# Optimization experiments

Hardware: AMD Instinct MI355X
Metric: run time of the kernel (lower is better)

## Reference

```python
import jax, jax.numpy as jnp
import numpy as np

NEG_SLOPE = 0.2  # PyG GATConv default LeakyReLU slope


def _gat_conv(x, edge_index, W, a_src, a_dst, bias, heads, out_dim, concat):
    """PyG-style GATConv (eval mode, add_self_loops=True).
    x: [N, F_in], edge_index: [2, E] (row=src, col=dst)."""
    N = x.shape[0]
    loops = jnp.tile(jnp.arange(N, dtype=edge_index.dtype)[None, :], (2, 1))
    ei = jnp.concatenate([edge_index, loops], axis=1)  # [2, E+N]
    src, dst = ei[0], ei[1]

    h = (x @ W).reshape(N, heads, out_dim)            # [N, H, D]
    alpha_s = jnp.einsum('nhd,hd->nh', h, a_src)       # [N, H]
    alpha_d = jnp.einsum('nhd,hd->nh', h, a_dst)       # [N, H]

    e = jax.nn.leaky_relu(alpha_s[src] + alpha_d[dst], NEG_SLOPE)  # [E', H]
    # segment softmax over edges grouped by destination node
    m = jax.ops.segment_max(e, dst, num_segments=N)
    e = jnp.exp(e - jax.lax.stop_gradient(m)[dst])
    denom = jax.ops.segment_sum(e, dst, num_segments=N)
    alpha = e / denom[dst]                              # [E', H]

    msg = h[src] * alpha[..., None]                     # [E', H, D]
    out = jax.ops.segment_sum(msg, dst, num_segments=N) # [N, H, D]
    out = out.reshape(N, heads * out_dim) if concat else out.mean(axis=1)
    return out + bias


def setup_inputs() -> dict:
    key = jax.random.key(0)
    ks = jax.random.split(key, 12)
    N, E, F_in, H, D = 50000, 1600000, 64, 2, 32
    s = 0.1
    return {
        'x': jax.random.normal(ks[0], (N, F_in), jnp.float32),
        'edge_index': jax.random.randint(ks[1], (2, E), 0, N, jnp.int64 if jax.config.jax_enable_x64 else jnp.int32),
        'W1': jax.random.normal(ks[2], (F_in, H * D), jnp.float32) * s,
        'a_src1': jax.random.normal(ks[3], (H, D), jnp.float32) * s,
        'a_dst1': jax.random.normal(ks[4], (H, D), jnp.float32) * s,
        'b1': jnp.zeros((H * D,), jnp.float32),
        'W2': jax.random.normal(ks[5], (H * D, D), jnp.float32) * s,
        'a_src2': jax.random.normal(ks[6], (1, D), jnp.float32) * s,
        'a_dst2': jax.random.normal(ks[7], (1, D), jnp.float32) * s,
        'b2': jnp.zeros((D,), jnp.float32),
        'fcW': jax.random.normal(ks[8], (D, 1), jnp.float32) * s,
        'fcb': jnp.zeros((1,), jnp.float32),
    }


def reference(x, edge_index, W1, a_src1, a_dst1, b1, W2, a_src2, a_dst2, b2, fcW, fcb):
    H, D = 2, 32
    h = _gat_conv(x, edge_index, W1, a_src1, a_dst1, b1, heads=H, out_dim=D, concat=True)
    h = jax.nn.elu(h)
    # dropout p=0.1 is a no-op in eval mode
    h = _gat_conv(h, edge_index, W2, a_src2, a_dst2, b2, heads=1, out_dim=D, concat=False)
    h = jax.nn.elu(h)
    scores = h @ fcW + fcb
    return (scores, h)
```

## Files before the change

### kernel.cpp

```cpp
#include <hip/hip_runtime.h>
#include <hip/hip_fp16.h>

#define NEG_SLOPE 0.2f
#define NRANGE 8
#define CAP 96

__device__ __forceinline__ float elu_f(float x) {
    return x > 0.f ? x : __expf(x) - 1.f;
}
__device__ __forceinline__ float lrelu_f(float x) {
    return fmaxf(x, NEG_SLOPE * x);
}

union H4 { float2 f2; __half2 h2[2]; };

__global__ __launch_bounds__(256) void scat_gemm1_kernel(
    const int* __restrict__ ei, int* __restrict__ cnt,
    unsigned short* __restrict__ srclist, int E, int N,
    int nScat, int nChunks,
    const float* __restrict__ x, const float* __restrict__ W1,
    const float* __restrict__ a_src, const float* __restrict__ a_dst,
    __half* __restrict__ h1, float* __restrict__ as1, float* __restrict__ ad1)
{
    __shared__ float Xl[4][64];
    int b = blockIdx.x;
    if (b < 7 * nScat && (b % 7) == 0) {
        int hid = b / 7;
        int range = hid & (NRANGE - 1);
        int chunk = hid >> 3;
        int RS = (N + NRANGE - 1) / NRANGE;
        int lo = range * RS;
        unsigned span = (unsigned)(((lo + RS) > N ? N : (lo + RS)) - lo);
        int per = (E + nChunks - 1) / nChunks;
        int beg = chunk * per;
        int end = beg + per; if (end > E) end = E;
        for (int i = beg + (int)threadIdx.x; i < end; i += 256) {
            int dst = ei[E + i];
            if ((unsigned)(dst - lo) < span) {
                int src = ei[i];
                int pos = atomicAdd(&cnt[dst], 1);
                srclist[(size_t)dst * CAP + pos] = (unsigned short)src;
            }
        }
        return;
    }
    int gid = (b < 7 * nScat) ? (b - b / 7 - 1) : (b - nScat);
    int tid = threadIdx.x;
    int r   = tid >> 6;
    int col = tid & 63;
    int row = gid * 4 + r;
    if (row < N) Xl[r][col] = x[(size_t)row * 64 + col];
    __syncthreads();
    if (row >= N) return;

    float acc = 0.f;
#pragma unroll
    for (int k = 0; k < 64; ++k) acc += Xl[r][k] * W1[k * 64 + col];
    h1[(size_t)row * 64 + col] = __float2half(acc);

    int head = col >> 5;
    float ps = acc * a_src[col];
    float pd = acc * a_dst[col];
#pragma unroll
    for (int off = 16; off; off >>= 1) {
        ps += __shfl_xor(ps, off, 32);
        pd += __shfl_xor(pd, off, 32);
    }
    if ((col & 31) == 0) {
        as1[row * 2 + head] = ps;
        ad1[row * 2 + head] = pd;
    }
}

__global__ __launch_bounds__(256) void agg1_gemm2_kernel(
    const int* __restrict__ dcnt, const unsigned short* __restrict__ srclist,
    const __half* __restrict__ h1, const float* __restrict__ as1,
    const float* __restrict__ ad1, const float* __restrict__ b1,
    const float* __restrict__ W2, const float* __restrict__ a_s2,
    const float* __restrict__ a_d2,
    __half* __restrict__ h2, float* __restrict__ as2, float* __restrict__ ad2,
    int N)
{
    __shared__ float W2l[64 * 32];
    __shared__ float sh[4][64];
    int tid = threadIdx.x;
    for (int i = tid; i < 64 * 32; i += 256) W2l[i] = W2[i];
    __syncthreads();

    int n = (blockIdx.x * 256 + tid) >> 6;
    int lane = tid & 63;
    int wid = tid >> 6;
    if (n >= N) return;

    int grp = lane >> 4;
    int cl  = lane & 15;
    int head = cl >> 3;
    float adn = ad1[n * 2 + head];
    const __half* h1q = h1 + 4 * cl;

    float den = 0.f, a0 = 0.f, a1 = 0.f, a2 = 0.f, a3 = 0.f;
    int beg = n * CAP;
    int deg = dcnt[n];
    int total = deg + 1;

    for (int base = 0; base < total; base += 64) {
        int rem = total - base;
        int cnt = rem > 64 ? 64 : rem;
        int li = base + lane;
        int es = (li < deg) ? (int)srclist[beg + li] : n;
        int j = 0;
        for (; j + 8 <= cnt; j += 8) {
            int sA = __shfl(es, j + grp, 64);
            int sB = __shfl(es, j + 4 + grp, 64);
            float aA = as1[sA * 2 + head];
            float aB = as1[sB * 2 + head];
            H4 uA, uB;
            uA.f2 = *(const float2*)(h1q + (size_t)sA * 64);
            uB.f2 = *(const float2*)(h1q + (size_t)sB * 64);
            float wA = __expf(lrelu_f(aA + adn));
            float wB = __expf(lrelu_f(aB + adn));
            float2 gA01 = __half22float2(uA.h2[0]);
            float2 gA23 = __half22float2(uA.h2[1]);
            float2 gB01 = __half22float2(uB.h2[0]);
            float2 gB23 = __half22float2(uB.h2[1]);
            den += wA + wB;
            a0 += wA * gA01.x + wB * gB01.x;
            a1 += wA * gA01.y + wB * gB01.y;
            a2 += wA * gA23.x + wB * gB23.x;
            a3 += wA * gA23.y + wB * gB23.y;
        }
        for (; j < cnt; j += 4) {
            int e = j + grp;
            int s = __shfl(es, e & 63, 64);
            float a = as1[s * 2 + head];
            H4 u;
            u.f2 = *(const float2*)(h1q + (size_t)s * 64);
            float w = (e < rem) ? __expf(lrelu_f(a + adn)) : 0.f;
            float2 g01 = __half22float2(u.h2[0]);
            float2 g23 = __half22float2(u.h2[1]);
            den += w;
            a0 += w * g01.x; a1 += w * g01.y;
            a2 += w * g23.x; a3 += w * g23.y;
        }
    }
    a0 += __shfl_xor(a0, 16, 64); a1 += __shfl_xor(a1, 16, 64);
    a2 += __shfl_xor(a2, 16, 64); a3 += __shfl_xor(a3, 16, 64);
    den += __shfl_xor(den, 16, 64);
    a0 += __shfl_xor(a0, 32, 64); a1 += __shfl_xor(a1, 32, 64);
    a2 += __shfl_xor(a2, 32, 64); a3 += __shfl_xor(a3, 32, 64);
    den += __shfl_xor(den, 32, 64);

    float4 bb = *(const float4*)(b1 + 4 * cl);
    float inv = 1.f / den;
    float v0 = elu_f(a0 * inv + bb.x);
    float v1 = elu_f(a1 * inv + bb.y);
    float v2 = elu_f(a2 * inv + bb.z);
    float v3 = elu_f(a3 * inv + bb.w);
    if (grp == 0) ((float4*)sh[wid])[cl] = make_float4(v0, v1, v2, v3);

    int col = lane & 31;
    int kbase = (lane >> 5) * 32;
    float p = 0.f;
#pragma unroll
    for (int jj = 0; jj < 32; ++jj)
        p += sh[wid][kbase + jj] * W2l[(kbase + jj) * 32 + col];
    p += __shfl_xor(p, 32, 64);

    if (lane < 32) h2[(size_t)n * 32 + lane] = __float2half(p);

    float ps = p * a_s2[col];
    float pd = p * a_d2[col];
#pragma unroll
    for (int off = 16; off; off >>= 1) {
        ps += __shfl_xor(ps, off, 32);
        pd += __shfl_xor(pd, off, 32);
    }
    if (lane == 0) { as2[n] = ps; ad2[n] = pd; }
}

__global__ __launch_bounds__(256) void agg2_kernel(
    const int* __restrict__ dcnt, const unsigned short* __restrict__ srclist,
    const __half* __restrict__ h2, const float* __restrict__ as2,
    const float* __restrict__ ad2, const float* __restrict__ b2,
    const float* __restrict__ fcW, const float* __restrict__ fcb,
    float* __restrict__ out, int N)
{
    int g = blockIdx.x * 256 + threadIdx.x;
    int n = g >> 5;
    if (n >= N) return;
    int l32 = g & 31;
    int grp = l32 >> 3;
    int cl  = l32 & 7;
    float adn = ad2[n];
    const __half* h2q = h2 + 4 * cl;

    float den = 0.f, a0 = 0.f, a1 = 0.f, a2 = 0.f, a3 = 0.f;
    int beg = n * CAP;
    int deg = dcnt[n];
    int total = deg + 1;

    for (int base = 0; base < total; base += 32) {
        int rem = total - base;
        int cnt = rem > 32 ? 32 : rem;
        int li = base + l32;
        int es = (li < deg) ? (int)srclist[beg + li] : n;
        int j = 0;
        for (; j + 8 <= cnt; j += 8) {
            int sA = __shfl(es, j + grp, 32);
            int sB = __shfl(es, j + 4 + grp, 32);
            float aA = as2[sA];
            float aB = as2[sB];
            H4 uA, uB;
            uA.f2 = *(const float2*)(h2q + (size_t)sA * 32);
            uB.f2 = *(const float2*)(h2q + (size_t)sB * 32);
            float wA = __expf(lrelu_f(aA + adn));
            float wB = __expf(lrelu_f(aB + adn));
            float2 gA01 = __half22float2(uA.h2[0]);
            float2 gA23 = __half22float2(uA.h2[1]);
            float2 gB01 = __half22float2(uB.h2[0]);
            float2 gB23 = __half22float2(uB.h2[1]);
            den += wA + wB;
            a0 += wA * gA01.x + wB * gB01.x;
            a1 += wA * gA01.y + wB * gB01.y;
            a2 += wA * gA23.x + wB * gB23.x;
            a3 += wA * gA23.y + wB * gB23.y;
        }
        for (; j < cnt; j += 4) {
            int e = j + grp;
            int s = __shfl(es, e & 31, 32);
            float a = as2[s];
            H4 u;
            u.f2 = *(const float2*)(h2q + (size_t)s * 32);
            float w = (e < rem) ? __expf(lrelu_f(a + adn)) : 0.f;
            float2 g01 = __half22float2(u.h2[0]);
            float2 g23 = __half22float2(u.h2[1]);
            den += w;
            a0 += w * g01.x; a1 += w * g01.y;
            a2 += w * g23.x; a3 += w * g23.y;
        }
    }
    a0 += __shfl_xor(a0, 8, 64);  a1 += __shfl_xor(a1, 8, 64);
    a2 += __shfl_xor(a2, 8, 64);  a3 += __shfl_xor(a3, 8, 64);
    den += __shfl_xor(den, 8, 64);
    a0 += __shfl_xor(a0, 16, 64); a1 += __shfl_xor(a1, 16, 64);
    a2 += __shfl_xor(a2, 16, 64); a3 += __shfl_xor(a3, 16, 64);
    den += __shfl_xor(den, 16, 64);

    float4 bb = *(const float4*)(b2 + 4 * cl);
    float inv = 1.f / den;
    float v0 = elu_f(a0 * inv + bb.x);
    float v1 = elu_f(a1 * inv + bb.y);
    float v2 = elu_f(a2 * inv + bb.z);
    float v3 = elu_f(a3 * inv + bb.w);
    if (grp == 0)
        ((float4*)(out + (size_t)N + (size_t)n * 32))[cl] =
            make_float4(v0, v1, v2, v3);

    float4 fw = *(const float4*)(fcW + 4 * cl);
    float p = v0 * fw.x + v1 * fw.y + v2 * fw.z + v3 * fw.w;
    p += __shfl_xor(p, 1, 64);
    p += __shfl_xor(p, 2, 64);
    p += __shfl_xor(p, 4, 64);
    if (l32 == 0) out[n] = p + fcb[0];
}

extern "C" void kernel_launch(void* const* d_in, const int* in_sizes, int n_in,
                              void* d_out, int out_size, void* d_ws, size_t ws_size,
                              hipStream_t stream) {
    const float* x    = (const float*)d_in[0];
    const int*   ei   = (const int*)d_in[1];
    const float* W1   = (const float*)d_in[2];
    const float* a_s1 = (const float*)d_in[3];
    const float* a_d1 = (const float*)d_in[4];
    const float* b1   = (const float*)d_in[5];
    const float* W2   = (const float*)d_in[6];
    const float* a_s2 = (const float*)d_in[7];
    const float* a_d2 = (const float*)d_in[8];
    const float* b2   = (const float*)d_in[9];
    const float* fcW  = (const float*)d_in[10];
    const float* fcb  = (const float*)d_in[11];

    const int N = in_sizes[0] / 64;
    const int E = in_sizes[1] / 2;

    float* fws  = (float*)d_ws;
    float* as1  = fws;
    float* ad1  = as1 + (size_t)2 * N;
    float* as2  = ad1 + (size_t)2 * N;
    float* ad2  = as2 + (size_t)N;
    __half* h2  = (__half*)(ad2 + (size_t)N);
    __half* h1  = h2 + (size_t)32 * N;
    int*   cnt  = (int*)(h1 + (size_t)64 * N);
    unsigned short* srclist = (unsigned short*)(cnt + N);

    hipMemsetAsync(cnt, 0, sizeof(int) * (size_t)N, stream);

    const int nChunks = 256;
    const int nScat = nChunks * NRANGE;
    const int nG1 = (N + 3) / 4;
    int extra = nG1 - 6 * nScat; if (extra < 0) extra = 0;
    scat_gemm1_kernel<<<7 * nScat + extra, 256, 0, stream>>>(
        ei, cnt, srclist, E, N, nScat, nChunks, x, W1, a_s1, a_d1, h1, as1, ad1);

    agg1_gemm2_kernel<<<((size_t)N * 64 + 255) / 256, 256, 0, stream>>>(
        cnt, srclist, h1, as1, ad1, b1, W2, a_s2, a_d2, h2, as2, ad2, N);

    agg2_kernel<<<((size_t)N * 32 + 255) / 256, 256, 0, stream>>>(
        cnt, srclist, h2, as2, ad2, b2, fcW, fcb, (float*)d_out, N);
}
```

Before: 238.2 us.

## Use shared-memory histogram two-pass CSR build and multi-node agg1 blocks

Scatter blocks now count destinations in an LDS histogram, reserve per-node slots with one global atomic per node, then place sources using LDS atomics. This cuts global atomic traffic. The scatter grid shrinks to 16 ranges by 8 chunks with vectorized int4 edge loads, so each scatter block reads a much larger chunk of edges. agg1_gemm2 now processes 4 nodes per wave per block, which amortizes the W2 shared-memory load, but it launches fewer blocks and the edge scan is now serialized within fewer scatter blocks.

```diff
diff --git a/kernel.cpp b/kernel.cpp
--- a/kernel.cpp
+++ b/kernel.cpp
@@ -2,7 +2,9 @@
 #include <hip/hip_fp16.h>
 
 #define NEG_SLOPE 0.2f
-#define NRANGE 8
+#define NRANGE 16
+#define NCHUNK 8
+#define HCAP 4096
 #define CAP 96
 
 __device__ __forceinline__ float elu_f(float x) {
@@ -17,35 +19,94 @@
 __global__ __launch_bounds__(256) void scat_gemm1_kernel(
     const int* __restrict__ ei, int* __restrict__ cnt,
     unsigned short* __restrict__ srclist, int E, int N,
-    int nScat, int nChunks,
+    int nScat, int nG1,
     const float* __restrict__ x, const float* __restrict__ W1,
     const float* __restrict__ a_src, const float* __restrict__ a_dst,
     __half* __restrict__ h1, float* __restrict__ as1, float* __restrict__ ad1)
 {
+    __shared__ int   hist[HCAP];
     __shared__ float Xl[4][64];
     int b = blockIdx.x;
-    if (b < 7 * nScat && (b % 7) == 0) {
-        int hid = b / 7;
+    int tid = threadIdx.x;
+    if (b < 17 * nScat && (b % 17) == 0) {
+        int hid = b / 17;
         int range = hid & (NRANGE - 1);
-        int chunk = hid >> 3;
+        int chunk = hid >> 4;
         int RS = (N + NRANGE - 1) / NRANGE;
         int lo = range * RS;
-        unsigned span = (unsigned)(((lo + RS) > N ? N : (lo + RS)) - lo);
-        int per = (E + nChunks - 1) / nChunks;
+        int hiN = lo + RS; if (hiN > N) hiN = N;
+        unsigned span = (unsigned)(hiN - lo);
+        int per = (((E + NCHUNK - 1) / NCHUNK) + 7) & ~7;
         int beg = chunk * per;
         int end = beg + per; if (end > E) end = E;
-        for (int i = beg + (int)threadIdx.x; i < end; i += 256) {
-            int dst = ei[E + i];
-            if ((unsigned)(dst - lo) < span) {
-                int src = ei[i];
-                int pos = atomicAdd(&cnt[dst], 1);
-                srclist[(size_t)dst * CAP + pos] = (unsigned short)src;
+
+        if (RS <= HCAP) {
+            for (int i = tid; i < RS; i += 256) hist[i] = 0;
+            __syncthreads();
+            if (beg < E) {
+                int nfull = (end - beg) >> 11;
+#define CNT1(dv) { unsigned r_ = (unsigned)((dv) - lo);                 \
+                   if (r_ < span) atomicAdd(&hist[r_], 1); }
+                for (int j = 0; j < nfull; ++j) {
+                    int i = beg + (j << 11) + tid * 8;
+                    int4 d0 = *(const int4*)(ei + E + i);
+                    int4 d1 = *(const int4*)(ei + E + i + 4);
+                    CNT1(d0.x); CNT1(d0.y); CNT1(d0.z); CNT1(d0.w);
+                    CNT1(d1.x); CNT1(d1.y); CNT1(d1.z); CNT1(d1.w);
+                }
+                for (int i = beg + (nfull << 11) + tid; i < end; i += 256) {
+                    int dv = ei[E + i];
+                    CNT1(dv);
+                }
+#undef CNT1
+            }
+            __syncthreads();
+            for (int i = tid; i < RS; i += 256) {
+                int c = hist[i];
+                if (c > 0) hist[i] = atomicAdd(&cnt[lo + i], c);
+            }
+            __syncthreads();
+            if (beg < E) {
+                int nfull = (end - beg) >> 11;
+#define PUT1(dv, sv) { unsigned r_ = (unsigned)((dv) - lo);             \
+                   if (r_ < span) {                                     \
+                       int pos_ = atomicAdd(&hist[r_], 1);              \
+                       srclist[(size_t)(dv) * CAP + pos_] =             \
+                           (unsigned short)(sv); } }
+                for (int j = 0; j < nfull; ++j) {
+                    int i = beg + (j << 11) + tid * 8;
+                    int4 d0 = *(const int4*)(ei + E + i);
+                    int4 d1 = *(const int4*)(ei + E + i + 4);
+                    int4 s0 = *(const int4*)(ei + i);
+                    int4 s1 = *(const int4*)(ei + i + 4);
+                    PUT1(d0.x, s0.x); PUT1(d0.y, s0.y);
+                    PUT1(d0.z, s0.z); PUT1(d0.w, s0.w);
+                    PUT1(d1.x, s1.x); PUT1(d1.y, s1.y);
+                    PUT1(d1.z, s1.z); PUT1(d1.w, s1.w);
+                }
+                for (int i = beg + (nfull << 11) + tid; i < end; i += 256) {
+                    int dv = ei[E + i];
+                    int sv = ei[i];
+                    PUT1(dv, sv);
+                }
+#undef PUT1
+            }
+        } else {
+            if (beg < E) {
+                for (int i = beg + tid; i < end; i += 256) {
+                    int dst = ei[E + i];
+                    if ((unsigned)(dst - lo) < span) {
+                        int src = ei[i];
+                        int pos = atomicAdd(&cnt[dst], 1);
+                        srclist[(size_t)dst * CAP + pos] = (unsigned short)src;
+                    }
+                }
             }
         }
         return;
     }
-    int gid = (b < 7 * nScat) ? (b - b / 7 - 1) : (b - nScat);
-    int tid = threadIdx.x;
+    int gid = (b < 17 * nScat) ? (b - b / 17 - 1) : (b - nScat);
+    if (gid >= nG1) return;
     int r   = tid >> 6;
     int col = tid & 63;
     int row = gid * 4 + r;
@@ -87,95 +148,97 @@
     for (int i = tid; i < 64 * 32; i += 256) W2l[i] = W2[i];
     __syncthreads();
 
-    int n = (blockIdx.x * 256 + tid) >> 6;
     int lane = tid & 63;
     int wid = tid >> 6;
-    if (n >= N) return;
-
     int grp = lane >> 4;
     int cl  = lane & 15;
     int head = cl >> 3;
-    float adn = ad1[n * 2 + head];
     const __half* h1q = h1 + 4 * cl;
 
-    float den = 0.f, a0 = 0.f, a1 = 0.f, a2 = 0.f, a3 = 0.f;
-    int beg = n * CAP;
-    int deg = dcnt[n];
-    int total = deg + 1;
-
-    for (int base = 0; base < total; base += 64) {
-        int rem = total - base;
-        int cnt = rem > 64 ? 64 : rem;
-        int li = base + lane;
-        int es = (li < deg) ? (int)srclist[beg + li] : n;
-        int j = 0;
-        for (; j + 8 <= cnt; j += 8) {
-            int sA = __shfl(es, j + grp, 64);
-            int sB = __shfl(es, j + 4 + grp, 64);
-            float aA = as1[sA * 2 + head];
-            float aB = as1[sB * 2 + head];
-            H4 uA, uB;
-            uA.f2 = *(const float2*)(h1q + (size_t)sA * 64);
-            uB.f2 = *(const float2*)(h1q + (size_t)sB * 64);
-            float wA = __expf(lrelu_f(aA + adn));
-            float wB = __expf(lrelu_f(aB + adn));
-            float2 gA01 = __half22float2(uA.h2[0]);
-            float2 gA23 = __half22float2(uA.h2[1]);
-            float2 gB01 = __half22float2(uB.h2[0]);
-            float2 gB23 = __half22float2(uB.h2[1]);
-            den += wA + wB;
-            a0 += wA * gA01.x + wB * gB01.x;
-            a1 += wA * gA01.y + wB * gB01.y;
-            a2 += wA * gA23.x + wB * gB23.x;
-            a3 += wA * gA23.y + wB * gB23.y;
-        }
-        for (; j < cnt; j += 4) {
-            int e = j + grp;
-            int s = __shfl(es, e & 63, 64);
-            float a = as1[s * 2 + head];
-            H4 u;
-            u.f2 = *(const float2*)(h1q + (size_t)s * 64);
-            float w = (e < rem) ? __expf(lrelu_f(a + adn)) : 0.f;
-            float2 g01 = __half22float2(u.h2[0]);
-            float2 g23 = __half22float2(u.h2[1]);
-            den += w;
-            a0 += w * g01.x; a1 += w * g01.y;
-            a2 += w * g23.x; a3 += w * g23.y;
-        }
-    }
-    a0 += __shfl_xor(a0, 16, 64); a1 += __shfl_xor(a1, 16, 64);
-    a2 += __shfl_xor(a2, 16, 64); a3 += __shfl_xor(a3, 16, 64);
-    den += __shfl_xor(den, 16, 64);
-    a0 += __shfl_xor(a0, 32, 64); a1 += __shfl_xor(a1, 32, 64);
-    a2 += __shfl_xor(a2, 32, 64); a3 += __shfl_xor(a3, 32, 64);
-    den += __shfl_xor(den, 32, 64);
-
-    float4 bb = *(const float4*)(b1 + 4 * cl);
-    float inv = 1.f / den;
-    float v0 = elu_f(a0 * inv + bb.x);
-    float v1 = elu_f(a1 * inv + bb.y);
-    float v2 = elu_f(a2 * inv + bb.z);
-    float v3 = elu_f(a3 * inv + bb.w);
-    if (grp == 0) ((float4*)sh[wid])[cl] = make_float4(v0, v1, v2, v3);
-
-    int col = lane & 31;
-    int kbase = (lane >> 5) * 32;
-    float p = 0.f;
+    for (int g = 0; g < 4; ++g) {
+        int n = (blockIdx.x * 4 + g) * 4 + wid;
+        if (n >= N) continue;
+        float adn = ad1[n * 2 + head];
+
+        float den = 0.f, a0 = 0.f, a1 = 0.f, a2 = 0.f, a3 = 0.f;
+        int beg = n * CAP;
+        int deg = dcnt[n];
+        int total = deg + 1;
+
+        for (int base = 0; base < total; base += 64) {
+            int rem = total - base;
+            int cnt = rem > 64 ? 64 : rem;
+            int li = base + lane;
+            int es = (li < deg) ? (int)srclist[beg + li] : n;
+            int j = 0;
+            for (; j + 8 <= cnt; j += 8) {
+                int sA = __shfl(es, j + grp, 64);
+                int sB = __shfl(es, j + 4 + grp, 64);
+                float aA = as1[sA * 2 + head];
+                float aB = as1[sB * 2 + head];
+                H4 uA, uB;
+                uA.f2 = *(const float2*)(h1q + (size_t)sA * 64);
+                uB.f2 = *(const float2*)(h1q + (size_t)sB * 64);
+                float wA = __expf(lrelu_f(aA + adn));
+                float wB = __expf(lrelu_f(aB + adn));
+                float2 gA01 = __half22float2(uA.h2[0]);
+                float2 gA23 = __half22float2(uA.h2[1]);
+                float2 gB01 = __half22float2(uB.h2[0]);
+                float2 gB23 = __half22float2(uB.h2[1]);
+                den += wA + wB;
+                a0 += wA * gA01.x + wB * gB01.x;
+                a1 += wA * gA01.y + wB * gB01.y;
+                a2 += wA * gA23.x + wB * gB23.x;
+                a3 += wA * gA23.y + wB * gB23.y;
+            }
+            for (; j < cnt; j += 4) {
+                int e = j + grp;
+                int s = __shfl(es, e & 63, 64);
+                float a = as1[s * 2 + head];
+                H4 u;
+                u.f2 = *(const float2*)(h1q + (size_t)s * 64);
+                float w = (e < rem) ? __expf(lrelu_f(a + adn)) : 0.f;
+                float2 g01 = __half22float2(u.h2[0]);
+                float2 g23 = __half22float2(u.h2[1]);
+                den += w;
+                a0 += w * g01.x; a1 += w * g01.y;
+                a2 += w * g23.x; a3 += w * g23.y;
+            }
+        }
+        a0 += __shfl_xor(a0, 16, 64); a1 += __shfl_xor(a1, 16, 64);
+        a2 += __shfl_xor(a2, 16, 64); a3 += __shfl_xor(a3, 16, 64);
+        den += __shfl_xor(den, 16, 64);
+        a0 += __shfl_xor(a0, 32, 64); a1 += __shfl_xor(a1, 32, 64);
+        a2 += __shfl_xor(a2, 32, 64); a3 += __shfl_xor(a3, 32, 64);
+        den += __shfl_xor(den, 32, 64);
+
+        float4 bb = *(const float4*)(b1 + 4 * cl);
+        float inv = 1.f / den;
+        float v0 = elu_f(a0 * inv + bb.x);
+        float v1 = elu_f(a1 * inv + bb.y);
+        float v2 = elu_f(a2 * inv + bb.z);
+        float v3 = elu_f(a3 * inv + bb.w);
+        if (grp == 0) ((float4*)sh[wid])[cl] = make_float4(v0, v1, v2, v3);
+
+        int col = lane & 31;
+        int kbase = (lane >> 5) * 32;
+        float p = 0.f;
 #pragma unroll
-    for (int jj = 0; jj < 32; ++jj)
-        p += sh[wid][kbase + jj] * W2l[(kbase + jj) * 32 + col];
-    p += __shfl_xor(p, 32, 64);
-
-    if (lane < 32) h2[(size_t)n * 32 + lane] = __float2half(p);
-
-    float ps = p * a_s2[col];
-    float pd = p * a_d2[col];
+        for (int jj = 0; jj < 32; ++jj)
+            p += sh[wid][kbase + jj] * W2l[(kbase + jj) * 32 + col];
+        p += __shfl_xor(p, 32, 64);
+
+        if (lane < 32) h2[(size_t)n * 32 + lane] = __float2half(p);
+
+        float ps = p * a_s2[col];
+        float pd = p * a_d2[col];
 #pragma unroll
-    for (int off = 16; off; off >>= 1) {
-        ps += __shfl_xor(ps, off, 32);
-        pd += __shfl_xor(pd, off, 32);
-    }
-    if (lane == 0) { as2[n] = ps; ad2[n] = pd; }
+        for (int off = 16; off; off >>= 1) {
+            ps += __shfl_xor(ps, off, 32);
+            pd += __shfl_xor(pd, off, 32);
+        }
+        if (lane == 0) { as2[n] = ps; ad2[n] = pd; }
+    }
 }
 
 __global__ __launch_bounds__(256) void agg2_kernel(
@@ -295,14 +358,15 @@
 
     hipMemsetAsync(cnt, 0, sizeof(int) * (size_t)N, stream);
 
-    const int nChunks = 256;
-    const int nScat = nChunks * NRANGE;
+    const int nScat = NRANGE * NCHUNK;
     const int nG1 = (N + 3) / 4;
-    int extra = nG1 - 6 * nScat; if (extra < 0) extra = 0;
-    scat_gemm1_kernel<<<7 * nScat + extra, 256, 0, stream>>>(
-        ei, cnt, srclist, E, N, nScat, nChunks, x, W1, a_s1, a_d1, h1, as1, ad1);
-
-    agg1_gemm2_kernel<<<((size_t)N * 64 + 255) / 256, 256, 0, stream>>>(
+    int grid = nG1 + nScat;
+    int minGrid = 17 * nScat;
+    if (grid < minGrid) grid = minGrid;
+    scat_gemm1_kernel<<<grid, 256, 0, stream>>>(
+        ei, cnt, srclist, E, N, nScat, nG1, x, W1, a_s1, a_d1, h1, as1, ad1);
+
+    agg1_gemm2_kernel<<<((size_t)N + 15) / 16, 256, 0, stream>>>(
         cnt, srclist, h1, as1, ad1, b1, W2, a_s2, a_d2, h2, as2, ad2, N);
 
     agg2_kernel<<<((size_t)N * 32 + 255) / 256, 256, 0, stream>>>(
```

Measured after the change: 333.4 us. +40.0%, slower.
